# Kernel optimization log

Hardware: AMD Instinct MI355X
Metric: run time of the kernel (lower is better)

The kernel has to match this reference:

```python
import jax, jax.numpy as jnp
import numpy as np

D_MODEL = 2560
D_INNER = 5120   # expand * d_model
D_STATE = 16
D_CONV = 4
DT_RANK = 160    # ceil(2560/16)
BATCH = 2
SEQ = 2048


def setup_inputs() -> dict:
    key = jax.random.key(0)
    ks = jax.random.split(key, 9)
    s = 0.02
    hidden_states = jax.random.normal(ks[0], (BATCH, SEQ, D_MODEL), jnp.float32)
    W_in = jax.random.normal(ks[1], (2 * D_INNER, D_MODEL), jnp.float32) * s
    conv_w = jax.random.normal(ks[2], (D_INNER, 1, D_CONV), jnp.float32) * s
    conv_b = jax.random.normal(ks[3], (D_INNER,), jnp.float32) * s
    W_x = jax.random.normal(ks[4], (DT_RANK + 2 * D_STATE, D_INNER), jnp.float32) * s
    W_dt = jax.random.normal(ks[5], (D_INNER, DT_RANK), jnp.float32) * s
    b_dt = jax.random.normal(ks[6], (D_INNER,), jnp.float32) * s
    A_log = jnp.log(jnp.arange(1, D_STATE + 1, dtype=jnp.float32))[None, :] * jnp.ones((D_INNER, 1), jnp.float32)
    D = jnp.ones((D_INNER,), jnp.float32)
    W_out = jax.random.normal(ks[7], (D_MODEL, D_INNER), jnp.float32) * s
    return {"hidden_states": hidden_states, "W_in": W_in, "conv_w": conv_w,
            "conv_b": conv_b, "W_x": W_x, "W_dt": W_dt, "b_dt": b_dt,
            "A_log": A_log, "D": D, "W_out": W_out}


def _mamba_forward(hidden_states, W_in, conv_w, conv_b, W_x, W_dt, b_dt, A_log, D, W_out):
    b, l, _ = hidden_states.shape
    # in_proj -> split x, z
    xz = jnp.einsum('bld,ed->ble', hidden_states, W_in)  # [B,L,2*d_inner]
    x, z = jnp.split(xz, 2, axis=-1)
    # causal depthwise conv1d (left pad d_conv-1, truncated to L)
    xc = jnp.transpose(x, (0, 2, 1))  # [B,C,L]
    xc = jax.lax.conv_general_dilated(
        xc, conv_w, window_strides=(1,), padding=[(D_CONV - 1, 0)],
        feature_group_count=D_INNER, dimension_numbers=('NCH', 'OIH', 'NCH'))
    xc = xc + conv_b[None, :, None]
    x = jax.nn.silu(jnp.transpose(xc, (0, 2, 1)))  # [B,L,d_inner]
    # x_proj -> dt_rank, B, C
    x_dbl = jnp.einsum('blc,ec->ble', x, W_x)
    dt_r = x_dbl[..., :DT_RANK]
    Bc = x_dbl[..., DT_RANK:DT_RANK + D_STATE]          # [B,L,n]
    Cc = x_dbl[..., DT_RANK + D_STATE:]                  # [B,L,n]
    # dt_proj (bias applied inside kernel via softplus) + time_step_limit [0, inf)
    dt = jnp.einsum('blr,cr->blc', dt_r, W_dt)
    dt = jax.nn.softplus(dt + b_dt)                      # [B,L,d_inner], >= 0
    A = -jnp.exp(A_log)                                  # [d_inner, n]

    # selective scan over time
    def step(h, inp):
        x_t, dt_t, B_t, C_t = inp  # [B,C],[B,C],[B,n],[B,n]
        dA = jnp.exp(dt_t[..., None] * A)                # [B,C,n]
        h = dA * h + (dt_t * x_t)[..., None] * B_t[:, None, :]
        y_t = jnp.sum(h * C_t[:, None, :], axis=-1)      # [B,C]
        return h, y_t

    h0 = jnp.zeros((b, D_INNER, D_STATE), x.dtype)
    xs = (jnp.transpose(x, (1, 0, 2)), jnp.transpose(dt, (1, 0, 2)),
          jnp.transpose(Bc, (1, 0, 2)), jnp.transpose(Cc, (1, 0, 2)))
    _, ys = jax.lax.scan(step, h0, xs)                   # [L,B,C]
    y = jnp.transpose(ys, (1, 0, 2)) + D * x             # [B,L,d_inner]
    # gate and out_proj (yoco_kv=False path: y * silu(z))
    y = y * jax.nn.silu(z)
    return jnp.einsum('blc,dc->bld', y, W_out)


def reference(hidden_states, W_in, conv_w, conv_b, W_x, W_dt, b_dt, A_log, D, W_out):
    return _mamba_forward(hidden_states, W_in, conv_w, conv_b, W_x, W_dt, b_dt, A_log, D, W_out)
```

## Files before the change

### kernel.cpp

```cpp
#include <hip/hip_runtime.h>
#include <math.h>

constexpr int kDM  = 2560;
constexpr int kDI  = 5120;
constexpr int kDS  = 16;
constexpr int kRK  = 160;
constexpr int kB   = 2;
constexpr int kL   = 2048;
constexpr int kBL  = kB * kL;
constexpr int kNXD = 256;
constexpr int kKDT = 192;
constexpr int kCH  = 64;
constexpr int kNCH = kL / kCH;

typedef _Float16 half8 __attribute__((ext_vector_type(8)));
typedef float    f32x4 __attribute__((ext_vector_type(4)));

__device__ __forceinline__ float fast_sigmoid(float x) { return 1.f / (1.f + __expf(-x)); }

__global__ __launch_bounds__(256)
void cvt_pad8(const float* __restrict__ src, _Float16* __restrict__ dst,
              long n8, int dcols8, int scols, int sstride, int srows)
{
    for (long i = blockIdx.x * 256L + threadIdx.x; i < n8; i += (long)gridDim.x * 256L) {
        const int r = (int)(i / dcols8);
        const int c = (int)(i - (long)r * dcols8) * 8;
        half8 v = {};
        if (r < srows && c < scols) {
            const float* s = src + (long)r * sstride + c;
            const float4 f0 = *(const float4*)s, f1 = *(const float4*)(s + 4);
            v[0]=(_Float16)f0.x; v[1]=(_Float16)f0.y; v[2]=(_Float16)f0.z; v[3]=(_Float16)f0.w;
            v[4]=(_Float16)f1.x; v[5]=(_Float16)f1.y; v[6]=(_Float16)f1.z; v[7]=(_Float16)f1.w;
        }
        *(half8*)(dst + i * 8) = v;
    }
}

template <int EPI>
__global__ __launch_bounds__(512, 2)
void gemm_big(const _Float16* __restrict__ A, const _Float16* __restrict__ B,
              void* C0, void* C1, int M, int N, int K, int nbx)
{
    __shared__ alignas(16) _Float16 lds[4 * 16384];
    const int tid  = threadIdx.x;
    const int wid  = tid >> 6;
    const int lane = tid & 63;
    const int wm = wid >> 2, wn = wid & 3;
    const int lr = lane & 15, lq = lane >> 4;
    const int xk = lr & 7;

    const int nwg = gridDim.x;
    int wg = blockIdx.x;
    wg = (wg & 7) * (nwg >> 3) + (wg >> 3);
    const int tM = (wg / nbx) * 256, tN = (wg % nbx) * 256;

    f32x4 acc[8][4] = {};

    const int scol = (((lane & 7) ^ (lane >> 3)) << 3);
    const int lrow = lane >> 3;
    const int NT = K >> 6;

    auto stageA = [&](int k0, int buf, int mh) {
        _Float16* dst = lds + buf * 32768;
#pragma unroll
        for (int round = 0; round < 2; ++round) {
            const int br = round * 128 + mh * 64 + wid * 8;
            const _Float16* src = A + (long)(tM + br + lrow) * K + k0 + scol;
            __builtin_amdgcn_global_load_lds(
                (const __attribute__((address_space(1))) void*)src,
                (__attribute__((address_space(3))) void*)(dst + br * 64), 16, 0, 0);
        }
    };
    auto stageB = [&](int k0, int buf, int nh) {
        _Float16* dst = lds + buf * 32768 + 16384;
#pragma unroll
        for (int round = 0; round < 2; ++round) {
            const int j = round * 8 + wid;
            const int br = (j >> 2) * 64 + nh * 32 + (j & 3) * 8;
            const _Float16* src = B + (long)(tN + br + lrow) * K + k0 + scol;
            __builtin_amdgcn_global_load_lds(
                (const __attribute__((address_space(1))) void*)src,
                (__attribute__((address_space(3))) void*)(dst + br * 64), 16, 0, 0);
        }
    };

    stageA(0, 0, 0); stageB(0, 0, 0); stageB(0, 0, 1); stageA(0, 0, 1);
    asm volatile("s_waitcnt vmcnt(0)" ::: "memory");
    asm volatile("s_barrier" ::: "memory");

    for (int t = 0; t < NT; ++t) {
        const int buf = t & 1;
        const _Float16* Asb = lds + buf * 32768;
        const _Float16* Bsb = Asb + 16384;
        const bool more = (t + 1 < NT);
        const int k1 = (t + 1) << 6;
#pragma unroll
        for (int p = 0; p < 4; ++p) {
            const int mh = p >> 1, nh = p & 1;
            half8 af[4][2], bf[2][2];
#pragma unroll
            for (int mi = 0; mi < 4; ++mi) {
                const _Float16* rp = Asb + (wm * 128 + mh * 64 + mi * 16 + lr) * 64;
#pragma unroll
                for (int kk = 0; kk < 2; ++kk)
                    af[mi][kk] = *(const half8*)(rp + (((kk * 4 + lq) ^ xk) << 3));
            }
#pragma unroll
            for (int ni = 0; ni < 2; ++ni) {
                const _Float16* rp = Bsb + (wn * 64 + nh * 32 + ni * 16 + lr) * 64;
#pragma unroll
                for (int kk = 0; kk < 2; ++kk)
                    bf[ni][kk] = *(const half8*)(rp + (((kk * 4 + lq) ^ xk) << 3));
            }
            if (more) {
                if (p == 0) {
                    stageA(k1, buf ^ 1, 0); stageB(k1, buf ^ 1, 0);
                    asm volatile("s_waitcnt vmcnt(4)" ::: "memory");
                } else if (p == 1) {
                    stageB(k1, buf ^ 1, 1); stageA(k1, buf ^ 1, 1);
                } else if (p == 3) {
                    asm volatile("s_waitcnt vmcnt(4)" ::: "memory");
                }
            } else {
                if (p == 0)
                    asm volatile("s_waitcnt vmcnt(0)" ::: "memory");
            }
            asm volatile("s_barrier" ::: "memory");
            __builtin_amdgcn_s_setprio(1);
#pragma unroll
            for (int mi = 0; mi < 4; ++mi)
#pragma unroll
                for (int ni = 0; ni < 2; ++ni)
#pragma unroll
                    for (int kk = 0; kk < 2; ++kk)
                        acc[mh * 4 + mi][nh * 2 + ni] =
                            __builtin_amdgcn_mfma_f32_16x16x32_f16(
                                af[mi][kk], bf[ni][kk],
                                acc[mh * 4 + mi][nh * 2 + ni], 0, 0, 0);
            __builtin_amdgcn_s_setprio(0);
            asm volatile("s_barrier" ::: "memory");
        }
    }

#pragma unroll
    for (int m = 0; m < 8; ++m) {
        const int row = tM + wm * 128 + m * 16 + lq * 4;
#pragma unroll
        for (int n = 0; n < 4; ++n) {
            const int col = tN + wn * 64 + n * 16 + lr;
#pragma unroll
            for (int j = 0; j < 4; ++j) {
                const float v = acc[m][n][j];
                if constexpr (EPI == 0) {
                    ((float*)C0)[(long)(row + j) * N + col] = v;
                } else {
                    if (col < kDI) ((_Float16*)C0)[(long)(row + j) * kDI + col] = (_Float16)v;
                    else           ((_Float16*)C1)[(long)(row + j) * kDI + (col - kDI)] = (_Float16)v;
                }
            }
        }
    }
}

template <int EPI>
__global__ __launch_bounds__(256)
void gemm_h(const _Float16* __restrict__ A, const _Float16* __restrict__ B,
            void* C0, void* C1, int M, int N, int K, int nbx,
            const float* __restrict__ bias)
{
    __shared__ alignas(16) _Float16 As[128 * 64];
    __shared__ alignas(16) _Float16 Bs[128 * 64];
    const int tid = threadIdx.x;
    const int w = tid >> 6, l = tid & 63;
    const int wr = w >> 1, wc = w & 1;
    const int nwg = gridDim.x;
    int wg = blockIdx.x;
    wg = (wg & 7) * (nwg >> 3) + (wg >> 3);
    const int tM = (wg / nbx) * 128, tN = (wg % nbx) * 128;

    f32x4 acc[4][4] = {};
    const int srow = l >> 3;
    const int scol = (l & 7) * 8;
    const _Float16* Ab = A + (long)tM * K + scol;
    const _Float16* Bb = B + (long)tN * K + scol;

    for (int k0 = 0; k0 < K; k0 += 64) {
#pragma unroll
        for (int i = 0; i < 4; ++i) {
            const int chunk = i * 4 + w;
            const int row = chunk * 8 + srow;
            __builtin_amdgcn_global_load_lds(
                (const __attribute__((address_space(1))) void*)(Ab + (long)row * K + k0),
                (__attribute__((address_space(3))) void*)(As + chunk * 512), 16, 0, 0);
            __builtin_amdgcn_global_load_lds(
                (const __attribute__((address_space(1))) void*)(Bb + (long)row * K + k0),
                (__attribute__((address_space(3))) void*)(Bs + chunk * 512), 16, 0, 0);
        }
        __syncthreads();

        const int lr = l & 15;
        const int lkb = (l >> 4) * 8;
#pragma unroll
        for (int kk = 0; kk < 2; ++kk) {
            const int lk = kk * 32 + lkb;
            half8 af[4], bf[4];
#pragma unroll
            for (int m = 0; m < 4; ++m)
                af[m] = *(const half8*)(As + (wr * 64 + m * 16 + lr) * 64 + lk);
#pragma unroll
            for (int n = 0; n < 4; ++n)
                bf[n] = *(const half8*)(Bs + (wc * 64 + n * 16 + lr) * 64 + lk);
#pragma unroll
            for (int m = 0; m < 4; ++m)
#pragma unroll
                for (int n = 0; n < 4; ++n)
                    acc[m][n] = __builtin_amdgcn_mfma_f32_16x16x32_f16(af[m], bf[n], acc[m][n], 0, 0, 0);
        }
        __syncthreads();
    }

    const int lr = l & 15, lq = l >> 4;
#pragma unroll
    for (int m = 0; m < 4; ++m) {
#pragma unroll
        for (int n = 0; n < 4; ++n) {
            const int col = tN + wc * 64 + n * 16 + lr;
            float bsv = 0.f;
            if constexpr (EPI == 1) bsv = bias[col];
#pragma unroll
            for (int j = 0; j < 4; ++j) {
                const int row = tM + wr * 64 + m * 16 + lq * 4 + j;
                float v = acc[m][n][j];
                if constexpr (EPI == 1) {
                    v += bsv;
                    v = (v > 20.f) ? v : log1pf(__expf(v));
                    ((_Float16*)C0)[(long)row * N + col] = (_Float16)v;
                } else {
                    ((float*)C0)[(long)row * N + col] = v;
                }
            }
        }
    }
}

__global__ __launch_bounds__(256)
void gemm_ks(const _Float16* __restrict__ A, const _Float16* __restrict__ B,
             float* __restrict__ C, int lda, int Kc)
{
    __shared__ alignas(16) _Float16 As[128 * 64];
    __shared__ alignas(16) _Float16 Bs[128 * 64];
    const int tid = threadIdx.x;
    const int w = tid >> 6, l = tid & 63;
    const int wr = w >> 1, wc = w & 1;
    const int nwg = gridDim.x;
    int wg = blockIdx.x;
    wg = (wg & 7) * (nwg >> 3) + (wg >> 3);
    const int tiles = nwg >> 2;
    const int s = wg / tiles, tile = wg - s * tiles;
    const int tM = (tile >> 1) * 128, tN = (tile & 1) * 128;

    f32x4 acc[4][4] = {};
    const int srow = l >> 3;
    const int scol = (l & 7) * 8;
    const _Float16* Ab = A + (long)tM * lda + s * Kc + scol;
    const _Float16* Bb = B + (long)tN * lda + s * Kc + scol;

    for (int k0 = 0; k0 < Kc; k0 += 64) {
#pragma unroll
        for (int i = 0; i < 4; ++i) {
            const int chunk = i * 4 + w;
            const int row = chunk * 8 + srow;
            __builtin_amdgcn_global_load_lds(
                (const __attribute__((address_space(1))) void*)(Ab + (long)row * lda + k0),
                (__attribute__((address_space(3))) void*)(As + chunk * 512), 16, 0, 0);
            __builtin_amdgcn_global_load_lds(
                (const __attribute__((address_space(1))) void*)(Bb + (long)row * lda + k0),
                (__attribute__((address_space(3))) void*)(Bs + chunk * 512), 16, 0, 0);
        }
        __syncthreads();

        const int lr = l & 15;
        const int lkb = (l >> 4) * 8;
#pragma unroll
        for (int kk = 0; kk < 2; ++kk) {
            const int lk = kk * 32 + lkb;
            half8 af[4], bf[4];
#pragma unroll
            for (int m = 0; m < 4; ++m)
                af[m] = *(const half8*)(As + (wr * 64 + m * 16 + lr) * 64 + lk);
#pragma unroll
            for (int n = 0; n < 4; ++n)
                bf[n] = *(const half8*)(Bs + (wc * 64 + n * 16 + lr) * 64 + lk);
#pragma unroll
            for (int m = 0; m < 4; ++m)
#pragma unroll
                for (int n = 0; n < 4; ++n)
                    acc[m][n] = __builtin_amdgcn_mfma_f32_16x16x32_f16(af[m], bf[n], acc[m][n], 0, 0, 0);
        }
        __syncthreads();
    }

    float* Cs = C + (long)s * kBL * kNXD;
    const int lr = l & 15, lq = l >> 4;
#pragma unroll
    for (int m = 0; m < 4; ++m)
#pragma unroll
        for (int n = 0; n < 4; ++n) {
            const int col = tN + wc * 64 + n * 16 + lr;
#pragma unroll
            for (int j = 0; j < 4; ++j) {
                const int row = tM + wr * 64 + m * 16 + lq * 4 + j;
                Cs[(long)row * kNXD + col] = acc[m][n][j];
            }
        }
}

__global__ __launch_bounds__(256)
void reduce4(const float* __restrict__ p, float* __restrict__ o)
{
    const long n4 = (long)kBL * kNXD / 4;
    for (long i = blockIdx.x * 256L + threadIdx.x; i < n4; i += (long)gridDim.x * 256L) {
        const f32x4 a = ((const f32x4*)p)[i];
        const f32x4 b = ((const f32x4*)p)[i + n4];
        const f32x4 c = ((const f32x4*)p)[i + 2 * n4];
        const f32x4 d = ((const f32x4*)p)[i + 3 * n4];
        ((f32x4*)o)[i] = (a + b) + (c + d);
    }
}

__global__ __launch_bounds__(256)
void conv_silu(const _Float16* __restrict__ x, const float* __restrict__ cw,
               const float* __restrict__ cb, _Float16* __restrict__ xs)
{
    const int c  = blockIdx.x * 256 + threadIdx.x;
    const int bl = blockIdx.y;
    const int l  = bl & (kL - 1);
    const long idx = (long)bl * kDI + c;
    const float4 wv = *(const float4*)(cw + c * 4);
    float acc = cb[c] + (float)x[idx] * wv.w;
    if (l >= 1) acc += (float)x[idx - kDI]     * wv.z;
    if (l >= 2) acc += (float)x[idx - 2 * kDI] * wv.y;
    if (l >= 3) acc += (float)x[idx - 3 * kDI] * wv.x;
    xs[idx] = (_Float16)(acc * fast_sigmoid(acc));
}

__global__ __launch_bounds__(256)
void scan_passA(const _Float16* __restrict__ dt, const _Float16* __restrict__ xs,
                const float* __restrict__ xdbl, const float* __restrict__ A_log,
                float* __restrict__ hend, float* __restrict__ pend)
{
    const int c  = blockIdx.x * 256 + threadIdx.x;
    const int ck = blockIdx.y, b = blockIdx.z;
    const int row0 = b * kL + ck * kCH;
    __shared__ float Bsh[kCH * kDS];
    for (int i = threadIdx.x; i < kCH * kDS; i += 256) {
        int t = i >> 4, s = i & 15;
        Bsh[i] = xdbl[(long)(row0 + t) * kNXD + kRK + s];
    }
    float Av[kDS];
#pragma unroll
    for (int s = 0; s < kDS; s += 4) {
        float4 v = *(const float4*)(A_log + (long)c * kDS + s);
        Av[s] = -__expf(v.x); Av[s+1] = -__expf(v.y); Av[s+2] = -__expf(v.z); Av[s+3] = -__expf(v.w);
    }
    __syncthreads();

    float h[kDS], P[kDS];
#pragma unroll
    for (int s = 0; s < kDS; ++s) { h[s] = 0.f; P[s] = 1.f; }
    const long base = (long)row0 * kDI + c;
    for (int t = 0; t < kCH; ++t) {
        const float dtv = (float)dt[base + (long)t * kDI];
        const float xv  = (float)xs[base + (long)t * kDI];
        const float dx = dtv * xv;
#pragma unroll
        for (int s = 0; s < kDS; ++s) {
            const float dA = __expf(dtv * Av[s]);
            h[s] = dA * h[s] + dx * Bsh[t * kDS + s];
            P[s] *= dA;
        }
    }
    const long o = ((long)(b * kNCH + ck) * kDI + c) * kDS;
#pragma unroll
    for (int s = 0; s < kDS; s += 4) {
        *(float4*)(hend + o + s) = make_float4(h[s], h[s+1], h[s+2], h[s+3]);
        *(float4*)(pend + o + s) = make_float4(P[s], P[s+1], P[s+2], P[s+3]);
    }
}

__global__ void scan_passB(float* hp, const float* __restrict__ pend)
{
    const long idx = blockIdx.x * 256L + threadIdx.x;
    const int  b   = (idx >= (long)kDI * kDS) ? 1 : 0;
    const long r   = idx - (long)b * kDI * kDS;
    float h = 0.f;
    for (int k = 0; k < kNCH; ++k) {
        const long o = ((long)(b * kNCH + k)) * ((long)kDI * kDS) + r;
        const float he = hp[o], pe = pend[o];
        hp[o] = h;
        h = fmaf(pe, h, he);
    }
}

__global__ __launch_bounds__(256)
void scan_passC(const _Float16* __restrict__ dt, const _Float16* xs,
                const float* __restrict__ xdbl, const float* __restrict__ A_log,
                const float* __restrict__ hin, const float* __restrict__ Dv,
                const _Float16* __restrict__ z, _Float16* yh)
{
    const int c  = blockIdx.x * 256 + threadIdx.x;
    const int ck = blockIdx.y, b = blockIdx.z;
    const int row0 = b * kL + ck * kCH;
    __shared__ float BC[kCH * 2 * kDS];
    for (int i = threadIdx.x; i < kCH * 2 * kDS; i += 256) {
        int t = i >> 5, s = i & 31;
        BC[i] = xdbl[(long)(row0 + t) * kNXD + kRK + s];
    }
    float Av[kDS];
#pragma unroll
    for (int s = 0; s < kDS; s += 4) {
        float4 v = *(const float4*)(A_log + (long)c * kDS + s);
        Av[s] = -__expf(v.x); Av[s+1] = -__expf(v.y); Av[s+2] = -__expf(v.z); Av[s+3] = -__expf(v.w);
    }
    __syncthreads();

    float h[kDS];
    const long oh = ((long)(b * kNCH + ck) * kDI + c) * kDS;
#pragma unroll
    for (int s = 0; s < kDS; s += 4) {
        float4 v = *(const float4*)(hin + oh + s);
        h[s] = v.x; h[s+1] = v.y; h[s+2] = v.z; h[s+3] = v.w;
    }
    const float dc = Dv[c];
    const long base = (long)row0 * kDI + c;
    for (int t = 0; t < kCH; ++t) {
        const long o = base + (long)t * kDI;
        const float dtv = (float)dt[o];
        const float xv  = (float)xs[o];
        const float zv  = (float)z[o];
        const float dx = dtv * xv;
        float y = dc * xv;
#pragma unroll
        for (int s = 0; s < kDS; ++s) {
            const float dA = __expf(dtv * Av[s]);
            h[s] = dA * h[s] + dx * BC[t * 32 + s];
            y += h[s] * BC[t * 32 + kDS + s];
        }
        yh[o] = (_Float16)(y * (zv * fast_sigmoid(zv)));
    }
}

extern "C" void kernel_launch(void* const* d_in, const int* in_sizes, int n_in,
                              void* d_out, int out_size, void* d_ws, size_t ws_size,
                              hipStream_t stream)
{
    const float* hidden = (const float*)d_in[0];
    const float* W_in   = (const float*)d_in[1];
    const float* conv_w = (const float*)d_in[2];
    const float* conv_b = (const float*)d_in[3];
    const float* W_x    = (const float*)d_in[4];
    const float* W_dt   = (const float*)d_in[5];
    const float* b_dt   = (const float*)d_in[6];
    const float* A_log  = (const float*)d_in[7];
    const float* Dvec   = (const float*)d_in[8];
    const float* W_out  = (const float*)d_in[9];
    float* out = (float*)d_out;
    (void)in_sizes; (void)n_in; (void)out_size; (void)ws_size;

    const size_t SZ    = (size_t)kBL * kDI * sizeof(_Float16);
    const size_t SZ_XD = (size_t)kBL * kNXD * sizeof(float);
    const size_t NST   = (size_t)kB * kNCH * kDI * kDS;
    char* ws = (char*)d_ws;
    _Float16* x_h   = (_Float16*)(ws);
    _Float16* z_h   = (_Float16*)(ws + SZ);
    _Float16* xs_h  = (_Float16*)(ws + 2 * SZ);
    float*    xdbl  = (float*)   (ws + 3 * SZ);
    float*    hend  = (float*)   (ws + 3 * SZ + SZ_XD);
    float*    pend  = hend + NST;
    _Float16* hid_h = (_Float16*)pend;
    _Float16* Win_h = xs_h;
    _Float16* Wx_h  = x_h;
    float*    xdp   = hend;
    _Float16* Wdt_h = (_Float16*)hend;
    _Float16* dtr_h = (_Float16*)((char*)hend + (2 << 20));
    _Float16* Wout_h= (_Float16*)hend;
    _Float16* dt_h  = x_h;
    _Float16* y_h   = xs_h;

    cvt_pad8<<<2048, 256, 0, stream>>>(hidden, hid_h, (long)kBL * kDM / 8, kDM / 8, kDM, kDM, kBL);
    cvt_pad8<<<2048, 256, 0, stream>>>(W_in, Win_h, (long)2 * kDI * kDM / 8, kDM / 8, kDM, kDM, 2 * kDI);

    gemm_big<2><<<(kBL / 256) * (2 * kDI / 256), 512, 0, stream>>>(
        hid_h, Win_h, x_h, z_h, kBL, 2 * kDI, kDM, 2 * kDI / 256);

    conv_silu<<<dim3(kDI / 256, kBL), 256, 0, stream>>>(x_h, conv_w, conv_b, xs_h);

    cvt_pad8<<<2048, 256, 0, stream>>>(W_x, Wx_h, (long)kNXD * kDI / 8, kDI / 8, kDI, kDI, kRK + 2 * kDS);

    gemm_ks<<<4 * (kBL / 128) * (kNXD / 128), 256, 0, stream>>>(xs_h, Wx_h, xdp, kDI, kDI / 4);
    reduce4<<<512, 256, 0, stream>>>(xdp, xdbl);

    cvt_pad8<<<2048, 256, 0, stream>>>(W_dt, Wdt_h, (long)kDI * kKDT / 8, kKDT / 8, kRK, kRK, kDI);
    cvt_pad8<<<2048, 256, 0, stream>>>(xdbl, dtr_h, (long)kBL * kKDT / 8, kKDT / 8, kRK, kNXD, kBL);

    gemm_h<1><<<(kDI / 128) * (kBL / 128), 256, 0, stream>>>(
        dtr_h, Wdt_h, dt_h, nullptr, kBL, kDI, kKDT, kDI / 128, b_dt);

    scan_passA<<<dim3(kDI / 256, kNCH, kB), 256, 0, stream>>>(dt_h, xs_h, xdbl, A_log, hend, pend);
    scan_passB<<<(kB * kDI * kDS) / 256, 256, 0, stream>>>(hend, pend);
    scan_passC<<<dim3(kDI / 256, kNCH, kB), 256, 0, stream>>>(dt_h, xs_h, xdbl, A_log, hend, Dvec, z_h, y_h);

    cvt_pad8<<<2048, 256, 0, stream>>>(W_out, Wout_h, (long)kDM * kDI / 8, kDI / 8, kDI, kDI, kDM);

    gemm_big<0><<<(kBL / 256) * (kDM / 256), 512, 0, stream>>>(
        y_h, Wout_h, out, nullptr, kBL, kDM, kDI, kDM / 256);
}
```

Baseline: 857.1 us.

## Reorder gemm_big sub-tile schedule to reuse fragments; use 128-tile GEMM for out_proj

The gemm_big inner loop now visits the four 64x32 sub-tiles in a serpentine order (A0B0, A0B1, A1B1, A1B0) and keeps the A and B fragments in registers between phases. This cuts LDS fragment reads per K-step roughly in half, at the cost of more live vector registers. Separately, the out_proj GEMM (M=4096, N=2560) moves from the 256x256 gemm_big kernel to the 128x128 gemm_h kernel. The grid grows from 160 to 640 workgroups, which should fill the CUs better than 160 large tiles do, but it loses the larger tile's data reuse.

Measured after the change: 896.8 us. +4.6%, slower.

```diff
diff --git a/kernel.cpp b/kernel.cpp
--- a/kernel.cpp
+++ b/kernel.cpp
@@ -48,6 +48,8 @@
     const int wm = wid >> 2, wn = wid & 3;
     const int lr = lane & 15, lq = lane >> 4;
     const int xk = lr & 7;
+    const int koff0 = ((lq ^ xk) << 3);
+    const int koff1 = (((4 + lq) ^ xk) << 3);
 
     const int nwg = gridDim.x;
     int wg = blockIdx.x;
@@ -94,52 +96,91 @@
         const _Float16* Bsb = Asb + 16384;
         const bool more = (t + 1 < NT);
         const int k1 = (t + 1) << 6;
-#pragma unroll
-        for (int p = 0; p < 4; ++p) {
-            const int mh = p >> 1, nh = p & 1;
-            half8 af[4][2], bf[2][2];
-#pragma unroll
-            for (int mi = 0; mi < 4; ++mi) {
-                const _Float16* rp = Asb + (wm * 128 + mh * 64 + mi * 16 + lr) * 64;
+        half8 af[4][2], bf0[2][2], bf1[2][2];
+
+#pragma unroll
+        for (int mi = 0; mi < 4; ++mi) {
+            const _Float16* rp = Asb + (wm * 128 + mi * 16 + lr) * 64;
+            af[mi][0] = *(const half8*)(rp + koff0);
+            af[mi][1] = *(const half8*)(rp + koff1);
+        }
+#pragma unroll
+        for (int ni = 0; ni < 2; ++ni) {
+            const _Float16* rp = Bsb + (wn * 64 + ni * 16 + lr) * 64;
+            bf0[ni][0] = *(const half8*)(rp + koff0);
+            bf0[ni][1] = *(const half8*)(rp + koff1);
+        }
+        if (more) {
+            stageA(k1, buf ^ 1, 0); stageB(k1, buf ^ 1, 0);
+            asm volatile("s_waitcnt vmcnt(4)" ::: "memory");
+        } else {
+            asm volatile("s_waitcnt vmcnt(0)" ::: "memory");
+        }
+        asm volatile("s_barrier" ::: "memory");
+        __builtin_amdgcn_s_setprio(1);
+#pragma unroll
+        for (int mi = 0; mi < 4; ++mi)
+#pragma unroll
+            for (int ni = 0; ni < 2; ++ni)
 #pragma unroll
                 for (int kk = 0; kk < 2; ++kk)
-                    af[mi][kk] = *(const half8*)(rp + (((kk * 4 + lq) ^ xk) << 3));
-            }
-#pragma unroll
-            for (int ni = 0; ni < 2; ++ni) {
-                const _Float16* rp = Bsb + (wn * 64 + nh * 32 + ni * 16 + lr) * 64;
+                    acc[mi][ni] = __builtin_amdgcn_mfma_f32_16x16x32_f16(
+                        af[mi][kk], bf0[ni][kk], acc[mi][ni], 0, 0, 0);
+        __builtin_amdgcn_s_setprio(0);
+        asm volatile("s_barrier" ::: "memory");
+
+#pragma unroll
+        for (int ni = 0; ni < 2; ++ni) {
+            const _Float16* rp = Bsb + (wn * 64 + 32 + ni * 16 + lr) * 64;
+            bf1[ni][0] = *(const half8*)(rp + koff0);
+            bf1[ni][1] = *(const half8*)(rp + koff1);
+        }
+        if (more) { stageB(k1, buf ^ 1, 1); stageA(k1, buf ^ 1, 1); }
+        asm volatile("s_barrier" ::: "memory");
+        __builtin_amdgcn_s_setprio(1);
+#pragma unroll
+        for (int mi = 0; mi < 4; ++mi)
+#pragma unroll
+            for (int ni = 0; ni < 2; ++ni)
 #pragma unroll
                 for (int kk = 0; kk < 2; ++kk)
-                    bf[ni][kk] = *(const half8*)(rp + (((kk * 4 + lq) ^ xk) << 3));
-            }
-            if (more) {
-                if (p == 0) {
-                    stageA(k1, buf ^ 1, 0); stageB(k1, buf ^ 1, 0);
-                    asm volatile("s_waitcnt vmcnt(4)" ::: "memory");
-                } else if (p == 1) {
-                    stageB(k1, buf ^ 1, 1); stageA(k1, buf ^ 1, 1);
-                } else if (p == 3) {
-                    asm volatile("s_waitcnt vmcnt(4)" ::: "memory");
-                }
-            } else {
-                if (p == 0)
-                    asm volatile("s_waitcnt vmcnt(0)" ::: "memory");
-            }
-            asm volatile("s_barrier" ::: "memory");
-            __builtin_amdgcn_s_setprio(1);
-#pragma unroll
-            for (int mi = 0; mi < 4; ++mi)
-#pragma unroll
-                for (int ni = 0; ni < 2; ++ni)
-#pragma unroll
-                    for (int kk = 0; kk < 2; ++kk)
-                        acc[mh * 4 + mi][nh * 2 + ni] =
-                            __builtin_amdgcn_mfma_f32_16x16x32_f16(
-                                af[mi][kk], bf[ni][kk],
-                                acc[mh * 4 + mi][nh * 2 + ni], 0, 0, 0);
-            __builtin_amdgcn_s_setprio(0);
-            asm volatile("s_barrier" ::: "memory");
-        }
+                    acc[mi][2 + ni] = __builtin_amdgcn_mfma_f32_16x16x32_f16(
+                        af[mi][kk], bf1[ni][kk], acc[mi][2 + ni], 0, 0, 0);
+        __builtin_amdgcn_s_setprio(0);
+        asm volatile("s_barrier" ::: "memory");
+
+#pragma unroll
+        for (int mi = 0; mi < 4; ++mi) {
+            const _Float16* rp = Asb + (wm * 128 + 64 + mi * 16 + lr) * 64;
+            af[mi][0] = *(const half8*)(rp + koff0);
+            af[mi][1] = *(const half8*)(rp + koff1);
+        }
+        asm volatile("s_barrier" ::: "memory");
+        __builtin_amdgcn_s_setprio(1);
+#pragma unroll
+        for (int mi = 0; mi < 4; ++mi)
+#pragma unroll
+            for (int ni = 0; ni < 2; ++ni)
+#pragma unroll
+                for (int kk = 0; kk < 2; ++kk)
+                    acc[4 + mi][2 + ni] = __builtin_amdgcn_mfma_f32_16x16x32_f16(
+                        af[mi][kk], bf1[ni][kk], acc[4 + mi][2 + ni], 0, 0, 0);
+        __builtin_amdgcn_s_setprio(0);
+        asm volatile("s_barrier" ::: "memory");
+
+        if (more) asm volatile("s_waitcnt vmcnt(4)" ::: "memory");
+        asm volatile("s_barrier" ::: "memory");
+        __builtin_amdgcn_s_setprio(1);
+#pragma unroll
+        for (int mi = 0; mi < 4; ++mi)
+#pragma unroll
+            for (int ni = 0; ni < 2; ++ni)
+#pragma unroll
+                for (int kk = 0; kk < 2; ++kk)
+                    acc[4 + mi][ni] = __builtin_amdgcn_mfma_f32_16x16x32_f16(
+                        af[mi][kk], bf0[ni][kk], acc[4 + mi][ni], 0, 0, 0);
+        __builtin_amdgcn_s_setprio(0);
+        asm volatile("s_barrier" ::: "memory");
     }
 
 #pragma unroll
@@ -512,6 +553,6 @@
 
     cvt_pad8<<<2048, 256, 0, stream>>>(W_out, Wout_h, (long)kDM * kDI / 8, kDI / 8, kDI, kDI, kDM);
 
-    gemm_big<0><<<(kBL / 256) * (kDM / 256), 512, 0, stream>>>(
-        y_h, Wout_h, out, nullptr, kBL, kDM, kDI, kDM / 256);
-}
+    gemm_h<0><<<(kDM / 128) * (kBL / 128), 256, 0, stream>>>(
+        y_h, Wout_h, out, nullptr, kBL, kDM, kDI, kDM / 128, nullptr);
+}
```
